# Kernel tuning notes

Measured on AMD Instinct MI355X. Metric: run time of the kernel, lower is better.

The kernel has to match this reference:

```python
import jax, jax.numpy as jnp
import numpy as np


def _block_causal_mask(cu_seqlens, seq_len):
    """Boolean [seq_len, seq_len] mask: True = attend (same doc AND causal)."""
    positions = jnp.arange(seq_len)
    # searchsorted(side='right') - 1 maps each position to its document id
    seq_ids = jnp.searchsorted(cu_seqlens, positions, side='right') - 1
    same_seq = seq_ids[:, None] == seq_ids[None, :]
    causal = positions[None, :] <= positions[:, None]
    return same_seq & causal


def setup_inputs() -> dict:
    key = jax.random.key(0)
    kq, kk, kv, kc = jax.random.split(key, 4)
    B, H, S, D = 1, 16, 4096, 128
    q = jax.random.normal(kq, (B, H, S, D), dtype=jnp.float32)
    k = jax.random.normal(kk, (B, H, S, D), dtype=jnp.float32)
    v = jax.random.normal(kv, (B, H, S, D), dtype=jnp.float32)
    # 8 packed documents: interior boundaries are sorted random ints in (0, S)
    inner = jnp.sort(jax.random.randint(kc, (7,), 1, S, dtype=jnp.int64))
    cu_seqlens = jnp.concatenate([
        jnp.zeros((1,), jnp.int64), inner, jnp.full((1,), S, jnp.int64)
    ])
    return {"q": q, "k": k, "v": v, "cu_seqlens": cu_seqlens, "max_seqlen": S}


def reference(q, k, v, cu_seqlens, max_seqlen):
    # q, k, v: [B, H, S, D]; block-diagonal causal SDPA over packed sequences.
    S, D = q.shape[2], q.shape[3]
    scale = 1.0 / jnp.sqrt(jnp.asarray(D, q.dtype))
    allow = _block_causal_mask(cu_seqlens, S)  # [S, S] bool
    scores = jnp.einsum('bhsd,bhtd->bhst', q, k) * scale  # [B, H, S, S]
    neg_inf = jnp.asarray(-jnp.inf, scores.dtype)
    scores = jnp.where(allow[None, None], scores, neg_inf)
    probs = jax.nn.softmax(scores, axis=-1)
    return jnp.einsum('bhst,bhtd->bhsd', probs, v)
```

## Files before the change

kernel.cpp:

```cpp
#include <hip/hip_runtime.h>

typedef float  f32x4  __attribute__((ext_vector_type(4)));
typedef __bf16 bf16x8 __attribute__((ext_vector_type(8)));
typedef unsigned short u16;
typedef u16 u16x8 __attribute__((ext_vector_type(8)));
typedef u16 u16x4 __attribute__((ext_vector_type(4)));
typedef unsigned u32x4 __attribute__((ext_vector_type(4)));

#define HEADS 16
#define DIM   128
#define QT    64
#define KTILE 64
#define PSTR  72
#define KSTR  136
#define VSTR  68

__device__ __forceinline__ u16 f2bf(float f) {
    unsigned u = __builtin_bit_cast(unsigned, f);
    u += 0x7FFFu + ((u >> 16) & 1u);
    return (u16)(u >> 16);
}

__device__ __forceinline__ void dma16(const void* g, void* l) {
    auto* gp = (const __attribute__((address_space(1))) unsigned*)(uintptr_t)g;
    auto* lp = (__attribute__((address_space(3))) unsigned*)(uintptr_t)l;
    __builtin_amdgcn_global_load_lds(gp, lp, 16, 0, 0);
}

__device__ __forceinline__ unsigned cvtpk(float lo, float hi) {
    unsigned r;
    asm("v_cvt_pk_bf16_f32 %0, %1, %2" : "=v"(r) : "v"(lo), "v"(hi));
    return r;
}

__global__ __launch_bounds__(256) void prep_kv(
    const float* __restrict__ K, const float* __restrict__ V,
    u16* __restrict__ KB, u16* __restrict__ VB, int S)
{
    __shared__ __align__(16) u16 T[128 * 72];
    int nt = S >> 6;
    int tile = blockIdx.x % nt, h = blockIdx.x / nt;
    int t = threadIdx.x;
    long tb = (long)(h * nt + tile) * 8192;

    const float* ksrc = K + ((long)(h * S + tile * 64)) * DIM;
#pragma unroll
    for (int it = 0; it < 4; ++it) {
        int idx = t + it * 256;
        int g = idx & 15, r = idx >> 4;
        const float* src = ksrc + (long)r * DIM + g * 8;
        f32x4 a = *(const f32x4*)src;
        f32x4 b = *(const f32x4*)(src + 4);
        u16x8 o;
        o[0]=f2bf(a[0]); o[1]=f2bf(a[1]); o[2]=f2bf(a[2]); o[3]=f2bf(a[3]);
        o[4]=f2bf(b[0]); o[5]=f2bf(b[1]); o[6]=f2bf(b[2]); o[7]=f2bf(b[3]);
        *(u16x8*)&KB[tb + r * 128 + ((g ^ (r & 7)) << 3)] = o;
    }

    int col4 = (t & 31) * 4;
    int row  = t >> 5;
    const float* vsrc = V + ((long)(h * S + tile * 64)) * DIM;
#pragma unroll
    for (int it = 0; it < 8; ++it) {
        int k = row + it * 8;
        f32x4 x = *(const f32x4*)(vsrc + (long)k * DIM + col4);
        T[(col4 + 0) * 72 + k] = f2bf(x[0]);
        T[(col4 + 1) * 72 + k] = f2bf(x[1]);
        T[(col4 + 2) * 72 + k] = f2bf(x[2]);
        T[(col4 + 3) * 72 + k] = f2bf(x[3]);
    }
    __syncthreads();
#pragma unroll
    for (int it = 0; it < 4; ++it) {
        int idx = t + it * 256;
        int d = idx >> 3, g2 = idx & 7;
        u16x8 o = *(const u16x8*)&T[d * 72 + g2 * 8];
        *(u16x8*)&VB[tb + d * 64 + ((g2 ^ (d & 7)) << 3)] = o;
    }
}

__global__ __launch_bounds__(256, 2) void fa_main(
    const float* __restrict__ Q, const u16* __restrict__ KB,
    const u16* __restrict__ VB, const void* __restrict__ cu_raw,
    int n_cu, float* __restrict__ O, int S, int n_qb)
{
    __shared__ __align__(16) u16 Kb[2][64 * 128];
    __shared__ __align__(16) u16 Vt[2][128 * 64];
    __shared__ __align__(16) u16 On[16 * 64];
    __shared__ int cu_s[32];

    const int tid  = threadIdx.x;
    const int wave = tid >> 6, lane = tid & 63;
    const int quad = lane >> 4, l16 = lane & 15;
    const int h  = blockIdx.x & (HEADS - 1);
    const int qb = (n_qb - 1) - (blockIdx.x >> 4);
    const int q0 = qb * QT;

    {
        const int* cu32 = (const int*)cu_raw;
        bool is64 = (cu32[1] == 0);
        for (int t = tid; t < n_cu; t += blockDim.x)
            cu_s[t] = is64 ? (int)((const long long*)cu_raw)[t] : cu32[t];
    }
    for (int i = tid; i < 1024; i += 256)
        On[i] = (i < 64) ? (u16)0x3F80 : (u16)0;
    __syncthreads();

    const float sc2 = 0.08838834764831845f * 1.4426950408889634f;
    const long hb = (long)h * S * DIM;
    const long hk = (long)h * (S >> 6) * 8192;
    const int qend = q0 + QT;

    const int qi_l = q0 + wave * 16 + l16;
    int qs = 0;
    for (int j = 0; j < n_cu; ++j) if (cu_s[j] <= qi_l) qs = cu_s[j];
    int q0s = 0;
    for (int j = 0; j < n_cu; ++j) if (cu_s[j] <= q0) q0s = cu_s[j];

    bf16x8 qfrag[4];
    {
        const float* qp = Q + hb + (long)(q0 + wave * 16 + l16) * DIM + quad * 8;
#pragma unroll
        for (int kk = 0; kk < 4; ++kk) {
            f32x4 x = *(const f32x4*)(qp + kk * 32);
            f32x4 y = *(const f32x4*)(qp + kk * 32 + 4);
            u16x8 u;
            u[0]=f2bf(x[0]); u[1]=f2bf(x[1]); u[2]=f2bf(x[2]); u[3]=f2bf(x[3]);
            u[4]=f2bf(y[0]); u[5]=f2bf(y[1]); u[6]=f2bf(y[2]); u[7]=f2bf(y[3]);
            qfrag[kk] = __builtin_bit_cast(bf16x8, u);
        }
    }

    f32x4 acc[9];
#pragma unroll
    for (int dt = 0; dt < 9; ++dt) acc[dt] = (f32x4){0.f, 0.f, 0.f, 0.f};

    const int t0 = (q0s & ~(KTILE - 1)) >> 6;
    const int ntile = (qend >> 6) - t0;
    const u16* ksrc = KB + hk;
    const u16* vsrc = VB + hk;

    {
        long off = (long)t0 * 8192;
#pragma unroll
        for (int c = 0; c < 4; ++c) {
            int ch = wave * 4 + c;
            dma16(ksrc + off + ch * 512 + lane * 8, &Kb[0][ch * 512]);
            dma16(vsrc + off + ch * 512 + lane * 8, &Vt[0][ch * 512]);
        }
    }

    for (int i = 0; i < ntile; ++i) {
        const int cur = i & 1;
        if (i + 1 < ntile) {
            long off = (long)(t0 + i + 1) * 8192;
#pragma unroll
            for (int c = 0; c < 4; ++c) {
                int ch = wave * 4 + c;
                dma16(ksrc + off + ch * 512 + lane * 8, &Kb[cur ^ 1][ch * 512]);
                dma16(vsrc + off + ch * 512 + lane * 8, &Vt[cur ^ 1][ch * 512]);
            }
            asm volatile("s_waitcnt vmcnt(8)" ::: "memory");
        } else {
            asm volatile("s_waitcnt vmcnt(0)" ::: "memory");
        }
        __builtin_amdgcn_s_barrier();

        const int kt = (t0 + i) << 6;
        const u16* kb = &Kb[cur][0];
        const u16* vt = &Vt[cur][0];

        f32x4 sc[4];
#pragma unroll
        for (int nt = 0; nt < 4; ++nt) sc[nt] = (f32x4){0.f, 0.f, 0.f, 0.f};
        __builtin_amdgcn_s_setprio(1);
#pragma unroll
        for (int kk = 0; kk < 4; ++kk)
#pragma unroll
            for (int nt = 0; nt < 4; ++nt) {
                int row = nt * 16 + l16;
                int g = kk * 4 + quad;
                u16x8 bu = *(const u16x8*)&kb[row * 128 + ((g ^ (row & 7)) << 3)];
                sc[nt] = __builtin_amdgcn_mfma_f32_16x16x32_bf16(
                    __builtin_bit_cast(bf16x8, bu), qfrag[kk], sc[nt], 0, 0, 0);
            }
        __builtin_amdgcn_s_setprio(0);

        float p[4][4];
#pragma unroll
        for (int nt = 0; nt < 4; ++nt) {
#pragma unroll
            for (int r = 0; r < 4; ++r) {
                int kj = kt + nt * 16 + quad * 4 + r;
                bool ok = (kj >= qs) && (kj <= qi_l);
                p[nt][r] = ok ? __builtin_amdgcn_exp2f(sc[nt][r] * sc2) : 0.f;
            }
        }

        unsigned Ra[4], Rb[4];
#pragma unroll
        for (int nt = 0; nt < 4; ++nt) {
            Ra[nt] = cvtpk(p[nt][0], p[nt][1]);
            Rb[nt] = cvtpk(p[nt][2], p[nt][3]);
        }

        __builtin_amdgcn_s_setprio(1);
#pragma unroll
        for (int kk2 = 0; kk2 < 2; ++kk2) {
            unsigned a0 = Ra[2*kk2], a1 = Ra[2*kk2 + 1];
            unsigned b0 = Rb[2*kk2], b1 = Rb[2*kk2 + 1];
            asm("v_permlane32_swap_b32 %0, %1" : "+v"(a0), "+v"(a1));
            asm("v_permlane16_swap_b32 %0, %1" : "+v"(a0), "+v"(a1));
            asm("v_permlane32_swap_b32 %0, %1" : "+v"(b0), "+v"(b1));
            asm("v_permlane16_swap_b32 %0, %1" : "+v"(b0), "+v"(b1));
            u32x4 wv; wv[0] = a0; wv[1] = b0; wv[2] = a1; wv[3] = b1;
            bf16x8 ap = __builtin_bit_cast(bf16x8, wv);

            int g2 = kk2 * 4 + quad;
#pragma unroll
            for (int dt = 0; dt < 8; ++dt) {
                int d = dt * 16 + l16;
                u16x8 bu = *(const u16x8*)&vt[(d << 6) + ((g2 ^ (d & 7)) << 3)];
                acc[dt] = __builtin_amdgcn_mfma_f32_16x16x32_bf16(
                    ap, __builtin_bit_cast(bf16x8, bu), acc[dt], 0, 0, 0);
            }
            {
                u16x8 bo = *(const u16x8*)&On[(l16 << 6) + ((g2 ^ (l16 & 7)) << 3)];
                acc[8] = __builtin_amdgcn_mfma_f32_16x16x32_bf16(
                    ap, __builtin_bit_cast(bf16x8, bo), acc[8], 0, 0, 0);
            }
        }
        __builtin_amdgcn_s_setprio(0);

        __builtin_amdgcn_s_barrier();
    }

#pragma unroll
    for (int r = 0; r < 4; ++r) {
        float l = __shfl(acc[8][r], (lane & 48), 64);
        int qi = q0 + wave * 16 + quad * 4 + r;
        float inv = 1.f / l;
        float* op = O + hb + (long)qi * DIM + l16;
#pragma unroll
        for (int dt = 0; dt < 8; ++dt)
            op[dt * 16] = acc[dt][r] * inv;
    }
}

__global__ __launch_bounds__(256, 2) void fa_fallback(
    const float* __restrict__ Q, const float* __restrict__ K,
    const float* __restrict__ V, const void* __restrict__ cu_raw,
    int n_cu, float* __restrict__ O, int S)
{
    __shared__ __align__(16) u16 Kb[KTILE * KSTR];
    __shared__ __align__(16) u16 Vt[DIM * VSTR];
    __shared__ __align__(16) u16 Pw[4][16 * PSTR];
    __shared__ int cu_s[32];

    const int tid  = threadIdx.x;
    const int wave = tid >> 6, lane = tid & 63;
    const int quad = lane >> 4, l16 = lane & 15;
    const int q0   = blockIdx.x * QT;
    const int h    = blockIdx.y;
    const int cg = tid & 31, rr = tid >> 5;
    const int dv = tid & 127, hiv = tid >> 7;

    {
        const int* cu32 = (const int*)cu_raw;
        bool is64 = (cu32[1] == 0);
        for (int t = tid; t < n_cu; t += blockDim.x)
            cu_s[t] = is64 ? (int)((const long long*)cu_raw)[t] : cu32[t];
    }
    __syncthreads();

    const long hb = (long)h * S * DIM;
    const float NEG_INF = -__builtin_inff();
    const float scale = 0.08838834764831845f;

    int qstart[4];
#pragma unroll
    for (int r = 0; r < 4; ++r) {
        int qi = q0 + wave * 16 + quad * 4 + r;
        int st = 0;
        for (int j = 0; j < n_cu; ++j) if (cu_s[j] <= qi) st = cu_s[j];
        qstart[r] = st;
    }
    int q0s = 0;
    for (int j = 0; j < n_cu; ++j) if (cu_s[j] <= q0) q0s = cu_s[j];

    bf16x8 qfrag[4];
    {
        const float* qp = Q + hb + (long)(q0 + wave * 16 + l16) * DIM + quad * 8;
#pragma unroll
        for (int kk = 0; kk < 4; ++kk) {
            f32x4 x = *(const f32x4*)(qp + kk * 32);
            f32x4 y = *(const f32x4*)(qp + kk * 32 + 4);
            u16x8 u;
            u[0]=f2bf(x[0]); u[1]=f2bf(x[1]); u[2]=f2bf(x[2]); u[3]=f2bf(x[3]);
            u[4]=f2bf(y[0]); u[5]=f2bf(y[1]); u[6]=f2bf(y[2]); u[7]=f2bf(y[3]);
            qfrag[kk] = __builtin_bit_cast(bf16x8, u);
        }
    }

    f32x4 acc[8];
#pragma unroll
    for (int dt = 0; dt < 8; ++dt) acc[dt] = (f32x4){0.f, 0.f, 0.f, 0.f};
    float m_r[4], l_r[4];
#pragma unroll
    for (int r = 0; r < 4; ++r) { m_r[r] = NEG_INF; l_r[r] = 0.f; }

    for (int kt = q0s & ~(KTILE - 1); kt < q0 + QT; kt += KTILE) {
        __syncthreads();
        {
#pragma unroll
            for (int it = 0; it < 8; ++it) {
                f32x4 kx = *(const f32x4*)(K + hb + (long)(kt + rr + it*8) * DIM + cg*4);
                u16x4 kb4;
                kb4[0]=f2bf(kx[0]); kb4[1]=f2bf(kx[1]);
                kb4[2]=f2bf(kx[2]); kb4[3]=f2bf(kx[3]);
                *(u16x4*)&Kb[(rr + it*8) * KSTR + cg*4] = kb4;
            }
#pragma unroll
            for (int p = 0; p < 8; ++p) {
                int kq = 2*p + hiv;
                const float* vp = V + hb + (long)(kt + kq*4) * DIM + dv;
                u16x4 w;
                w[0]=f2bf(vp[0]); w[1]=f2bf(vp[(long)DIM]);
                w[2]=f2bf(vp[(long)2*DIM]); w[3]=f2bf(vp[(long)3*DIM]);
                *(u16x4*)&Vt[dv * VSTR + kq*4] = w;
            }
        }
        __syncthreads();

        f32x4 sc[4];
#pragma unroll
        for (int nt = 0; nt < 4; ++nt) sc[nt] = (f32x4){0.f, 0.f, 0.f, 0.f};
#pragma unroll
        for (int kk = 0; kk < 4; ++kk)
#pragma unroll
            for (int nt = 0; nt < 4; ++nt) {
                u16x8 bu = *(const u16x8*)&Kb[(nt*16 + l16) * KSTR + kk*32 + quad*8];
                sc[nt] = __builtin_amdgcn_mfma_f32_16x16x32_bf16(
                    qfrag[kk], __builtin_bit_cast(bf16x8, bu), sc[nt], 0, 0, 0);
            }
#pragma unroll
        for (int nt = 0; nt < 4; ++nt) {
            int kj = kt + nt * 16 + l16;
#pragma unroll
            for (int r = 0; r < 4; ++r) {
                int qi = q0 + wave * 16 + quad * 4 + r;
                bool ok = (kj >= qstart[r]) && (kj <= qi);
                sc[nt][r] = ok ? sc[nt][r] * scale : NEG_INF;
            }
        }
        float mnew[4], alpha[4], rsum[4];
#pragma unroll
        for (int r = 0; r < 4; ++r) {
            float tm = fmaxf(fmaxf(sc[0][r], sc[1][r]), fmaxf(sc[2][r], sc[3][r]));
#pragma unroll
            for (int off = 1; off < 16; off <<= 1)
                tm = fmaxf(tm, __shfl_xor(tm, off, 64));
            float mn = fmaxf(m_r[r], tm);
            mnew[r]  = mn;
            alpha[r] = (mn == NEG_INF) ? 1.f : __expf(m_r[r] - mn);
            rsum[r]  = 0.f;
        }
#pragma unroll
        for (int nt = 0; nt < 4; ++nt)
#pragma unroll
            for (int r = 0; r < 4; ++r) {
                float pv = (sc[nt][r] == NEG_INF) ? 0.f : __expf(sc[nt][r] - mnew[r]);
                sc[nt][r] = pv;
                rsum[r] += pv;
            }
#pragma unroll
        for (int r = 0; r < 4; ++r) {
            float s = rsum[r];
#pragma unroll
            for (int off = 1; off < 16; off <<= 1) s += __shfl_xor(s, off, 64);
            l_r[r] = l_r[r] * alpha[r] + s;
            m_r[r] = mnew[r];
        }
#pragma unroll
        for (int dt = 0; dt < 8; ++dt)
#pragma unroll
            for (int r = 0; r < 4; ++r) acc[dt][r] *= alpha[r];

#pragma unroll
        for (int nt = 0; nt < 4; ++nt)
#pragma unroll
            for (int r = 0; r < 4; ++r)
                Pw[wave][(quad*4 + r) * PSTR + ((nt ^ quad) * 16 + l16)] = f2bf(sc[nt][r]);

#pragma unroll
        for (int kk2 = 0; kk2 < 2; ++kk2) {
            int colx = (kk2*32 + quad*8) ^ ((l16 >> 2) << 4);
            u16x8 au = *(const u16x8*)&Pw[wave][l16 * PSTR + colx];
            bf16x8 ap = __builtin_bit_cast(bf16x8, au);
#pragma unroll
            for (int dt = 0; dt < 8; ++dt) {
                int base = (dt*16 + l16) * VSTR + kk2*32 + quad*8;
                u16x4 lo = *(const u16x4*)&Vt[base];
                u16x4 hi = *(const u16x4*)&Vt[base + 4];
                u16x8 bu;
                bu[0]=lo[0]; bu[1]=lo[1]; bu[2]=lo[2]; bu[3]=lo[3];
                bu[4]=hi[0]; bu[5]=hi[1]; bu[6]=hi[2]; bu[7]=hi[3];
                acc[dt] = __builtin_amdgcn_mfma_f32_16x16x32_bf16(
                    ap, __builtin_bit_cast(bf16x8, bu), acc[dt], 0, 0, 0);
            }
        }
    }

#pragma unroll
    for (int r = 0; r < 4; ++r) {
        int qi = q0 + wave * 16 + quad * 4 + r;
        float inv = 1.f / l_r[r];
        float* op = O + hb + (long)qi * DIM + l16;
#pragma unroll
        for (int dt = 0; dt < 8; ++dt)
            op[dt * 16] = acc[dt][r] * inv;
    }
}

extern "C" void kernel_launch(void* const* d_in, const int* in_sizes, int n_in,
                              void* d_out, int out_size, void* d_ws, size_t ws_size,
                              hipStream_t stream) {
    const float* q = (const float*)d_in[0];
    const float* k = (const float*)d_in[1];
    const float* v = (const float*)d_in[2];
    const void* cu = d_in[3];
    int n_cu = in_sizes[3];
    int S = in_sizes[0] / (HEADS * DIM);
    size_t perMat = (size_t)HEADS * S * 256;
    if (ws_size >= 2 * perMat) {
        u16* KB = (u16*)d_ws;
        u16* VB = (u16*)((char*)d_ws + perMat);
        prep_kv<<<dim3(HEADS * (S >> 6)), 256, 0, stream>>>(k, v, KB, VB, S);
        int n_qb = S / QT;
        fa_main<<<dim3(n_qb * HEADS), 256, 0, stream>>>(
            q, KB, VB, cu, n_cu, (float*)d_out, S, n_qb);
    } else {
        fa_fallback<<<dim3(S / QT, HEADS), 256, 0, stream>>>(
            q, k, v, cu, n_cu, (float*)d_out, S);
    }
}
```

Measured before the change: 174.8 us.

## Double query tile per block to reuse K/V tiles across two row groups

Each wave now handles two 16-row query groups (128 query rows per block), so every K and V fragment read from LDS feeds two MFMAs instead of one. This halves K/V staging per query row and the number of blocks. Blocks are remapped so each of the 8 XCDs gets a fixed pair of heads, which should improve L2 locality. The row-sum ones matrix moves from LDS into a register constant. Costs are higher register pressure, fewer blocks (512) for load balance across the causal triangle, and a coarser causal start tile.

Result: slower. 187.6 us (+7.3%).

```diff
diff --git a/kernel.cpp b/kernel.cpp
--- a/kernel.cpp
+++ b/kernel.cpp
@@ -9,6 +9,7 @@
 
 #define HEADS 16
 #define DIM   128
+#define QTM   128
 #define QT    64
 #define KTILE 64
 #define PSTR  72
@@ -86,15 +87,26 @@
 {
     __shared__ __align__(16) u16 Kb[2][64 * 128];
     __shared__ __align__(16) u16 Vt[2][128 * 64];
-    __shared__ __align__(16) u16 On[16 * 64];
     __shared__ int cu_s[32];
 
     const int tid  = threadIdx.x;
     const int wave = tid >> 6, lane = tid & 63;
     const int quad = lane >> 4, l16 = lane & 15;
-    const int h  = blockIdx.x & (HEADS - 1);
-    const int qb = (n_qb - 1) - (blockIdx.x >> 4);
-    const int q0 = qb * QT;
+
+    int h, qb;
+    {
+        int total = n_qb * HEADS;
+        int bid = blockIdx.x;
+        if ((total & 7) == 0) {
+            int xcd = bid & 7, j = bid >> 3;
+            h  = xcd * (HEADS >> 3) + (j & ((HEADS >> 3) - 1));
+            qb = (n_qb - 1) - (j >> 1);
+        } else {
+            h  = bid & (HEADS - 1);
+            qb = (n_qb - 1) - (bid / HEADS);
+        }
+    }
+    const int q0 = qb * QTM;
 
     {
         const int* cu32 = (const int*)cu_raw;
@@ -102,24 +114,28 @@
         for (int t = tid; t < n_cu; t += blockDim.x)
             cu_s[t] = is64 ? (int)((const long long*)cu_raw)[t] : cu32[t];
     }
-    for (int i = tid; i < 1024; i += 256)
-        On[i] = (i < 64) ? (u16)0x3F80 : (u16)0;
     __syncthreads();
 
     const float sc2 = 0.08838834764831845f * 1.4426950408889634f;
     const long hb = (long)h * S * DIM;
     const long hk = (long)h * (S >> 6) * 8192;
-    const int qend = q0 + QT;
-
-    const int qi_l = q0 + wave * 16 + l16;
-    int qs = 0;
-    for (int j = 0; j < n_cu; ++j) if (cu_s[j] <= qi_l) qs = cu_s[j];
+    const int qend = q0 + QTM;
+
+    int qi_l[2], qs[2];
+#pragma unroll
+    for (int m = 0; m < 2; ++m) {
+        qi_l[m] = q0 + wave * 32 + m * 16 + l16;
+        int st = 0;
+        for (int j = 0; j < n_cu; ++j) if (cu_s[j] <= qi_l[m]) st = cu_s[j];
+        qs[m] = st;
+    }
     int q0s = 0;
     for (int j = 0; j < n_cu; ++j) if (cu_s[j] <= q0) q0s = cu_s[j];
 
-    bf16x8 qfrag[4];
-    {
-        const float* qp = Q + hb + (long)(q0 + wave * 16 + l16) * DIM + quad * 8;
+    bf16x8 qfrag[2][4];
+#pragma unroll
+    for (int m = 0; m < 2; ++m) {
+        const float* qp = Q + hb + (long)qi_l[m] * DIM + quad * 8;
 #pragma unroll
         for (int kk = 0; kk < 4; ++kk) {
             f32x4 x = *(const f32x4*)(qp + kk * 32);
@@ -127,13 +143,24 @@
             u16x8 u;
             u[0]=f2bf(x[0]); u[1]=f2bf(x[1]); u[2]=f2bf(x[2]); u[3]=f2bf(x[3]);
             u[4]=f2bf(y[0]); u[5]=f2bf(y[1]); u[6]=f2bf(y[2]); u[7]=f2bf(y[3]);
-            qfrag[kk] = __builtin_bit_cast(bf16x8, u);
-        }
-    }
-
-    f32x4 acc[9];
-#pragma unroll
-    for (int dt = 0; dt < 9; ++dt) acc[dt] = (f32x4){0.f, 0.f, 0.f, 0.f};
+            qfrag[m][kk] = __builtin_bit_cast(bf16x8, u);
+        }
+    }
+
+    bf16x8 ones;
+    {
+        u16 ov = (l16 == 0) ? (u16)0x3F80 : (u16)0;
+        u16x8 ou;
+#pragma unroll
+        for (int j = 0; j < 8; ++j) ou[j] = ov;
+        ones = __builtin_bit_cast(bf16x8, ou);
+    }
+
+    f32x4 acc[2][9];
+#pragma unroll
+    for (int m = 0; m < 2; ++m)
+#pragma unroll
+        for (int dt = 0; dt < 9; ++dt) acc[m][dt] = (f32x4){0.f, 0.f, 0.f, 0.f};
 
     const int t0 = (q0s & ~(KTILE - 1)) >> 6;
     const int ntile = (qend >> 6) - t0;
@@ -170,9 +197,11 @@
         const u16* kb = &Kb[cur][0];
         const u16* vt = &Vt[cur][0];
 
-        f32x4 sc[4];
-#pragma unroll
-        for (int nt = 0; nt < 4; ++nt) sc[nt] = (f32x4){0.f, 0.f, 0.f, 0.f};
+        f32x4 sc[2][4];
+#pragma unroll
+        for (int m = 0; m < 2; ++m)
+#pragma unroll
+            for (int nt = 0; nt < 4; ++nt) sc[m][nt] = (f32x4){0.f, 0.f, 0.f, 0.f};
         __builtin_amdgcn_s_setprio(1);
 #pragma unroll
         for (int kk = 0; kk < 4; ++kk)
@@ -181,54 +210,62 @@
                 int row = nt * 16 + l16;
                 int g = kk * 4 + quad;
                 u16x8 bu = *(const u16x8*)&kb[row * 128 + ((g ^ (row & 7)) << 3)];
-                sc[nt] = __builtin_amdgcn_mfma_f32_16x16x32_bf16(
-                    __builtin_bit_cast(bf16x8, bu), qfrag[kk], sc[nt], 0, 0, 0);
+                bf16x8 kf = __builtin_bit_cast(bf16x8, bu);
+                sc[0][nt] = __builtin_amdgcn_mfma_f32_16x16x32_bf16(
+                    kf, qfrag[0][kk], sc[0][nt], 0, 0, 0);
+                sc[1][nt] = __builtin_amdgcn_mfma_f32_16x16x32_bf16(
+                    kf, qfrag[1][kk], sc[1][nt], 0, 0, 0);
             }
         __builtin_amdgcn_s_setprio(0);
 
-        float p[4][4];
-#pragma unroll
-        for (int nt = 0; nt < 4; ++nt) {
-#pragma unroll
-            for (int r = 0; r < 4; ++r) {
-                int kj = kt + nt * 16 + quad * 4 + r;
-                bool ok = (kj >= qs) && (kj <= qi_l);
-                p[nt][r] = ok ? __builtin_amdgcn_exp2f(sc[nt][r] * sc2) : 0.f;
-            }
-        }
-
-        unsigned Ra[4], Rb[4];
-#pragma unroll
-        for (int nt = 0; nt < 4; ++nt) {
-            Ra[nt] = cvtpk(p[nt][0], p[nt][1]);
-            Rb[nt] = cvtpk(p[nt][2], p[nt][3]);
-        }
+        unsigned Ra[2][4], Rb[2][4];
+#pragma unroll
+        for (int m = 0; m < 2; ++m)
+#pragma unroll
+            for (int nt = 0; nt < 4; ++nt) {
+                int kjb = kt + nt * 16 + quad * 4;
+                float p0 = (kjb + 0 >= qs[m] && kjb + 0 <= qi_l[m])
+                               ? __builtin_amdgcn_exp2f(sc[m][nt][0] * sc2) : 0.f;
+                float p1 = (kjb + 1 >= qs[m] && kjb + 1 <= qi_l[m])
+                               ? __builtin_amdgcn_exp2f(sc[m][nt][1] * sc2) : 0.f;
+                float p2 = (kjb + 2 >= qs[m] && kjb + 2 <= qi_l[m])
+                               ? __builtin_amdgcn_exp2f(sc[m][nt][2] * sc2) : 0.f;
+                float p3 = (kjb + 3 >= qs[m] && kjb + 3 <= qi_l[m])
+                               ? __builtin_amdgcn_exp2f(sc[m][nt][3] * sc2) : 0.f;
+                Ra[m][nt] = cvtpk(p0, p1);
+                Rb[m][nt] = cvtpk(p2, p3);
+            }
 
         __builtin_amdgcn_s_setprio(1);
 #pragma unroll
         for (int kk2 = 0; kk2 < 2; ++kk2) {
-            unsigned a0 = Ra[2*kk2], a1 = Ra[2*kk2 + 1];
-            unsigned b0 = Rb[2*kk2], b1 = Rb[2*kk2 + 1];
-            asm("v_permlane32_swap_b32 %0, %1" : "+v"(a0), "+v"(a1));
-            asm("v_permlane16_swap_b32 %0, %1" : "+v"(a0), "+v"(a1));
-            asm("v_permlane32_swap_b32 %0, %1" : "+v"(b0), "+v"(b1));
-            asm("v_permlane16_swap_b32 %0, %1" : "+v"(b0), "+v"(b1));
-            u32x4 wv; wv[0] = a0; wv[1] = b0; wv[2] = a1; wv[3] = b1;
-            bf16x8 ap = __builtin_bit_cast(bf16x8, wv);
-
+            bf16x8 ap[2];
+#pragma unroll
+            for (int m = 0; m < 2; ++m) {
+                unsigned a0 = Ra[m][2*kk2], a1 = Ra[m][2*kk2 + 1];
+                unsigned b0 = Rb[m][2*kk2], b1 = Rb[m][2*kk2 + 1];
+                asm("v_permlane32_swap_b32 %0, %1" : "+v"(a0), "+v"(a1));
+                asm("v_permlane16_swap_b32 %0, %1" : "+v"(a0), "+v"(a1));
+                asm("v_permlane32_swap_b32 %0, %1" : "+v"(b0), "+v"(b1));
+                asm("v_permlane16_swap_b32 %0, %1" : "+v"(b0), "+v"(b1));
+                u32x4 wv; wv[0] = a0; wv[1] = b0; wv[2] = a1; wv[3] = b1;
+                ap[m] = __builtin_bit_cast(bf16x8, wv);
+            }
             int g2 = kk2 * 4 + quad;
 #pragma unroll
             for (int dt = 0; dt < 8; ++dt) {
                 int d = dt * 16 + l16;
                 u16x8 bu = *(const u16x8*)&vt[(d << 6) + ((g2 ^ (d & 7)) << 3)];
-                acc[dt] = __builtin_amdgcn_mfma_f32_16x16x32_bf16(
-                    ap, __builtin_bit_cast(bf16x8, bu), acc[dt], 0, 0, 0);
-            }
-            {
-                u16x8 bo = *(const u16x8*)&On[(l16 << 6) + ((g2 ^ (l16 & 7)) << 3)];
-                acc[8] = __builtin_amdgcn_mfma_f32_16x16x32_bf16(
-                    ap, __builtin_bit_cast(bf16x8, bo), acc[8], 0, 0, 0);
-            }
+                bf16x8 vf = __builtin_bit_cast(bf16x8, bu);
+                acc[0][dt] = __builtin_amdgcn_mfma_f32_16x16x32_bf16(
+                    ap[0], vf, acc[0][dt], 0, 0, 0);
+                acc[1][dt] = __builtin_amdgcn_mfma_f32_16x16x32_bf16(
+                    ap[1], vf, acc[1][dt], 0, 0, 0);
+            }
+            acc[0][8] = __builtin_amdgcn_mfma_f32_16x16x32_bf16(
+                ap[0], ones, acc[0][8], 0, 0, 0);
+            acc[1][8] = __builtin_amdgcn_mfma_f32_16x16x32_bf16(
+                ap[1], ones, acc[1][8], 0, 0, 0);
         }
         __builtin_amdgcn_s_setprio(0);
 
@@ -236,14 +273,16 @@
     }
 
 #pragma unroll
+    for (int m = 0; m < 2; ++m)
+#pragma unroll
     for (int r = 0; r < 4; ++r) {
-        float l = __shfl(acc[8][r], (lane & 48), 64);
-        int qi = q0 + wave * 16 + quad * 4 + r;
+        float l = __shfl(acc[m][8][r], (lane & 48), 64);
+        int qi = q0 + wave * 32 + m * 16 + quad * 4 + r;
         float inv = 1.f / l;
         float* op = O + hb + (long)qi * DIM + l16;
 #pragma unroll
         for (int dt = 0; dt < 8; ++dt)
-            op[dt * 16] = acc[dt][r] * inv;
+            op[dt * 16] = acc[m][dt][r] * inv;
     }
 }
 
@@ -432,11 +471,11 @@
     int n_cu = in_sizes[3];
     int S = in_sizes[0] / (HEADS * DIM);
     size_t perMat = (size_t)HEADS * S * 256;
-    if (ws_size >= 2 * perMat) {
+    if (ws_size >= 2 * perMat && (S % QTM) == 0) {
         u16* KB = (u16*)d_ws;
         u16* VB = (u16*)((char*)d_ws + perMat);
         prep_kv<<<dim3(HEADS * (S >> 6)), 256, 0, stream>>>(k, v, KB, VB, S);
-        int n_qb = S / QT;
+        int n_qb = S / QTM;
         fa_main<<<dim3(n_qb * HEADS), 256, 0, stream>>>(
             q, KB, VB, cu, n_cu, (float*)d_out, S, n_qb);
     } else {
```

## Single-buffer V, drop On LDS table, skip masked tiles, remap blocks per XCD

Applied to the files above, without the earlier changes.

V is now single-buffered in LDS and the LDS row-sum table is replaced with a register 'ones' fragment. Together these cut shared memory so the launch bound can rise to 3 blocks per CU. The V load for the next tile is issued after the barrier, so only K stays double-buffered. Waves skip the compute for tiles entirely outside their document/causal range. The block-to-(head, q-block) mapping is remapped so each XCD handles two heads, which should improve L2 locality. The trade-off is that V loads are less overlapped with compute.

New measurement: 179.3 us. 1.03x slower.

```diff
diff --git a/kernel.cpp b/kernel.cpp
--- a/kernel.cpp
+++ b/kernel.cpp
@@ -79,21 +79,32 @@
     }
 }
 
-__global__ __launch_bounds__(256, 2) void fa_main(
+__global__ __launch_bounds__(256, 3) void fa_main(
     const float* __restrict__ Q, const u16* __restrict__ KB,
     const u16* __restrict__ VB, const void* __restrict__ cu_raw,
     int n_cu, float* __restrict__ O, int S, int n_qb)
 {
     __shared__ __align__(16) u16 Kb[2][64 * 128];
-    __shared__ __align__(16) u16 Vt[2][128 * 64];
-    __shared__ __align__(16) u16 On[16 * 64];
+    __shared__ __align__(16) u16 Vt[128 * 64];
     __shared__ int cu_s[32];
 
     const int tid  = threadIdx.x;
     const int wave = tid >> 6, lane = tid & 63;
     const int quad = lane >> 4, l16 = lane & 15;
-    const int h  = blockIdx.x & (HEADS - 1);
-    const int qb = (n_qb - 1) - (blockIdx.x >> 4);
+
+    int h, qb;
+    {
+        int bid = blockIdx.x;
+        int total = n_qb * HEADS;
+        if ((total & 15) == 0) {
+            int xcd = bid & 7, j = bid >> 3;
+            h  = xcd * 2 + (j & 1);
+            qb = (n_qb - 1) - (j >> 1);
+        } else {
+            h  = bid & (HEADS - 1);
+            qb = (n_qb - 1) - (bid >> 4);
+        }
+    }
     const int q0 = qb * QT;
 
     {
@@ -102,8 +113,6 @@
         for (int t = tid; t < n_cu; t += blockDim.x)
             cu_s[t] = is64 ? (int)((const long long*)cu_raw)[t] : cu32[t];
     }
-    for (int i = tid; i < 1024; i += 256)
-        On[i] = (i < 64) ? (u16)0x3F80 : (u16)0;
     __syncthreads();
 
     const float sc2 = 0.08838834764831845f * 1.4426950408889634f;
@@ -117,9 +126,12 @@
     int q0s = 0;
     for (int j = 0; j < n_cu; ++j) if (cu_s[j] <= q0) q0s = cu_s[j];
 
+    const int wqmin = __builtin_amdgcn_readfirstlane(qs);
+    const int wqmax = q0 + wave * 16 + 15;
+
     bf16x8 qfrag[4];
     {
-        const float* qp = Q + hb + (long)(q0 + wave * 16 + l16) * DIM + quad * 8;
+        const float* qp = Q + hb + (long)qi_l * DIM + quad * 8;
 #pragma unroll
         for (int kk = 0; kk < 4; ++kk) {
             f32x4 x = *(const f32x4*)(qp + kk * 32);
@@ -131,6 +143,15 @@
         }
     }
 
+    bf16x8 ones;
+    {
+        u16 ov = (l16 == 0) ? (u16)0x3F80 : (u16)0;
+        u16x8 ou;
+#pragma unroll
+        for (int j = 0; j < 8; ++j) ou[j] = ov;
+        ones = __builtin_bit_cast(bf16x8, ou);
+    }
+
     f32x4 acc[9];
 #pragma unroll
     for (int dt = 0; dt < 9; ++dt) acc[dt] = (f32x4){0.f, 0.f, 0.f, 0.f};
@@ -146,7 +167,7 @@
         for (int c = 0; c < 4; ++c) {
             int ch = wave * 4 + c;
             dma16(ksrc + off + ch * 512 + lane * 8, &Kb[0][ch * 512]);
-            dma16(vsrc + off + ch * 512 + lane * 8, &Vt[0][ch * 512]);
+            dma16(vsrc + off + ch * 512 + lane * 8, &Vt[ch * 512]);
         }
     }
 
@@ -158,81 +179,84 @@
             for (int c = 0; c < 4; ++c) {
                 int ch = wave * 4 + c;
                 dma16(ksrc + off + ch * 512 + lane * 8, &Kb[cur ^ 1][ch * 512]);
-                dma16(vsrc + off + ch * 512 + lane * 8, &Vt[cur ^ 1][ch * 512]);
-            }
-            asm volatile("s_waitcnt vmcnt(8)" ::: "memory");
+            }
+            asm volatile("s_waitcnt vmcnt(4)" ::: "memory");
         } else {
             asm volatile("s_waitcnt vmcnt(0)" ::: "memory");
         }
         __builtin_amdgcn_s_barrier();
 
         const int kt = (t0 + i) << 6;
-        const u16* kb = &Kb[cur][0];
-        const u16* vt = &Vt[cur][0];
-
-        f32x4 sc[4];
-#pragma unroll
-        for (int nt = 0; nt < 4; ++nt) sc[nt] = (f32x4){0.f, 0.f, 0.f, 0.f};
-        __builtin_amdgcn_s_setprio(1);
-#pragma unroll
-        for (int kk = 0; kk < 4; ++kk)
+        if (kt <= wqmax && kt + KTILE > wqmin) {
+            const u16* kb = &Kb[cur][0];
+
+            f32x4 sc[4];
+#pragma unroll
+            for (int nt = 0; nt < 4; ++nt) sc[nt] = (f32x4){0.f, 0.f, 0.f, 0.f};
+            __builtin_amdgcn_s_setprio(1);
+#pragma unroll
+            for (int kk = 0; kk < 4; ++kk)
+#pragma unroll
+                for (int nt = 0; nt < 4; ++nt) {
+                    int row = nt * 16 + l16;
+                    int g = kk * 4 + quad;
+                    u16x8 bu = *(const u16x8*)&kb[row * 128 + ((g ^ (row & 7)) << 3)];
+                    sc[nt] = __builtin_amdgcn_mfma_f32_16x16x32_bf16(
+                        __builtin_bit_cast(bf16x8, bu), qfrag[kk], sc[nt], 0, 0, 0);
+                }
+            __builtin_amdgcn_s_setprio(0);
+
+            unsigned Ra[4], Rb[4];
 #pragma unroll
             for (int nt = 0; nt < 4; ++nt) {
-                int row = nt * 16 + l16;
-                int g = kk * 4 + quad;
-                u16x8 bu = *(const u16x8*)&kb[row * 128 + ((g ^ (row & 7)) << 3)];
-                sc[nt] = __builtin_amdgcn_mfma_f32_16x16x32_bf16(
-                    __builtin_bit_cast(bf16x8, bu), qfrag[kk], sc[nt], 0, 0, 0);
-            }
-        __builtin_amdgcn_s_setprio(0);
-
-        float p[4][4];
-#pragma unroll
-        for (int nt = 0; nt < 4; ++nt) {
-#pragma unroll
-            for (int r = 0; r < 4; ++r) {
-                int kj = kt + nt * 16 + quad * 4 + r;
-                bool ok = (kj >= qs) && (kj <= qi_l);
-                p[nt][r] = ok ? __builtin_amdgcn_exp2f(sc[nt][r] * sc2) : 0.f;
-            }
-        }
-
-        unsigned Ra[4], Rb[4];
-#pragma unroll
-        for (int nt = 0; nt < 4; ++nt) {
-            Ra[nt] = cvtpk(p[nt][0], p[nt][1]);
-            Rb[nt] = cvtpk(p[nt][2], p[nt][3]);
-        }
-
-        __builtin_amdgcn_s_setprio(1);
-#pragma unroll
-        for (int kk2 = 0; kk2 < 2; ++kk2) {
-            unsigned a0 = Ra[2*kk2], a1 = Ra[2*kk2 + 1];
-            unsigned b0 = Rb[2*kk2], b1 = Rb[2*kk2 + 1];
-            asm("v_permlane32_swap_b32 %0, %1" : "+v"(a0), "+v"(a1));
-            asm("v_permlane16_swap_b32 %0, %1" : "+v"(a0), "+v"(a1));
-            asm("v_permlane32_swap_b32 %0, %1" : "+v"(b0), "+v"(b1));
-            asm("v_permlane16_swap_b32 %0, %1" : "+v"(b0), "+v"(b1));
-            u32x4 wv; wv[0] = a0; wv[1] = b0; wv[2] = a1; wv[3] = b1;
-            bf16x8 ap = __builtin_bit_cast(bf16x8, wv);
-
-            int g2 = kk2 * 4 + quad;
-#pragma unroll
-            for (int dt = 0; dt < 8; ++dt) {
-                int d = dt * 16 + l16;
-                u16x8 bu = *(const u16x8*)&vt[(d << 6) + ((g2 ^ (d & 7)) << 3)];
-                acc[dt] = __builtin_amdgcn_mfma_f32_16x16x32_bf16(
-                    ap, __builtin_bit_cast(bf16x8, bu), acc[dt], 0, 0, 0);
-            }
-            {
-                u16x8 bo = *(const u16x8*)&On[(l16 << 6) + ((g2 ^ (l16 & 7)) << 3)];
+                int kjb = kt + nt * 16 + quad * 4;
+                float p0 = (kjb + 0 >= qs && kjb + 0 <= qi_l)
+                               ? __builtin_amdgcn_exp2f(sc[nt][0] * sc2) : 0.f;
+                float p1 = (kjb + 1 >= qs && kjb + 1 <= qi_l)
+                               ? __builtin_amdgcn_exp2f(sc[nt][1] * sc2) : 0.f;
+                float p2 = (kjb + 2 >= qs && kjb + 2 <= qi_l)
+                               ? __builtin_amdgcn_exp2f(sc[nt][2] * sc2) : 0.f;
+                float p3 = (kjb + 3 >= qs && kjb + 3 <= qi_l)
+                               ? __builtin_amdgcn_exp2f(sc[nt][3] * sc2) : 0.f;
+                Ra[nt] = cvtpk(p0, p1);
+                Rb[nt] = cvtpk(p2, p3);
+            }
+
+            __builtin_amdgcn_s_setprio(1);
+#pragma unroll
+            for (int kk2 = 0; kk2 < 2; ++kk2) {
+                unsigned a0 = Ra[2*kk2], a1 = Ra[2*kk2 + 1];
+                unsigned b0 = Rb[2*kk2], b1 = Rb[2*kk2 + 1];
+                asm("v_permlane32_swap_b32 %0, %1" : "+v"(a0), "+v"(a1));
+                asm("v_permlane16_swap_b32 %0, %1" : "+v"(a0), "+v"(a1));
+                asm("v_permlane32_swap_b32 %0, %1" : "+v"(b0), "+v"(b1));
+                asm("v_permlane16_swap_b32 %0, %1" : "+v"(b0), "+v"(b1));
+                u32x4 wv; wv[0] = a0; wv[1] = b0; wv[2] = a1; wv[3] = b1;
+                bf16x8 ap = __builtin_bit_cast(bf16x8, wv);
+
+                int g2 = kk2 * 4 + quad;
+#pragma unroll
+                for (int dt = 0; dt < 8; ++dt) {
+                    int d = dt * 16 + l16;
+                    u16x8 bu = *(const u16x8*)&Vt[(d << 6) + ((g2 ^ (d & 7)) << 3)];
+                    acc[dt] = __builtin_amdgcn_mfma_f32_16x16x32_bf16(
+                        ap, __builtin_bit_cast(bf16x8, bu), acc[dt], 0, 0, 0);
+                }
                 acc[8] = __builtin_amdgcn_mfma_f32_16x16x32_bf16(
-                    ap, __builtin_bit_cast(bf16x8, bo), acc[8], 0, 0, 0);
-            }
-        }
-        __builtin_amdgcn_s_setprio(0);
+                    ap, ones, acc[8], 0, 0, 0);
+            }
+            __builtin_amdgcn_s_setprio(0);
+        }
 
         __builtin_amdgcn_s_barrier();
+        if (i + 1 < ntile) {
+            long off = (long)(t0 + i + 1) * 8192;
+#pragma unroll
+            for (int c = 0; c < 4; ++c) {
+                int ch = wave * 4 + c;
+                dma16(vsrc + off + ch * 512 + lane * 8, &Vt[ch * 512]);
+            }
+        }
     }
 
 #pragma unroll
```

## Interleave QK MFMA with exp2 masking and hold ones-vector in registers

Applied to the files above, without the earlier changes.

Reorders the QK^T loop so that each 16-column score tile is finished first, then computes the exp2, mask and bf16 pack for the previous tile while the next tile's MFMAs issue. This overlaps transcendental and VALU work with matrix ops. It also replaces the LDS-resident ones matrix used for the row-sum MFMA with a register constant, which removes an LDS read per step and the LDS allocation. The mask check becomes a single unsigned range compare. The softmax has no max subtraction, so the accuracy behaviour is unchanged.

Result: no change. 172.0 us (-1.6%).

```diff
diff --git a/kernel.cpp b/kernel.cpp
--- a/kernel.cpp
+++ b/kernel.cpp
@@ -86,7 +86,6 @@
 {
     __shared__ __align__(16) u16 Kb[2][64 * 128];
     __shared__ __align__(16) u16 Vt[2][128 * 64];
-    __shared__ __align__(16) u16 On[16 * 64];
     __shared__ int cu_s[32];
 
     const int tid  = threadIdx.x;
@@ -102,8 +101,6 @@
         for (int t = tid; t < n_cu; t += blockDim.x)
             cu_s[t] = is64 ? (int)((const long long*)cu_raw)[t] : cu32[t];
     }
-    for (int i = tid; i < 1024; i += 256)
-        On[i] = (i < 64) ? (u16)0x3F80 : (u16)0;
     __syncthreads();
 
     const float sc2 = 0.08838834764831845f * 1.4426950408889634f;
@@ -116,10 +113,11 @@
     for (int j = 0; j < n_cu; ++j) if (cu_s[j] <= qi_l) qs = cu_s[j];
     int q0s = 0;
     for (int j = 0; j < n_cu; ++j) if (cu_s[j] <= q0) q0s = cu_s[j];
+    const int drange = qi_l - qs;
 
     bf16x8 qfrag[4];
     {
-        const float* qp = Q + hb + (long)(q0 + wave * 16 + l16) * DIM + quad * 8;
+        const float* qp = Q + hb + (long)qi_l * DIM + quad * 8;
 #pragma unroll
         for (int kk = 0; kk < 4; ++kk) {
             f32x4 x = *(const f32x4*)(qp + kk * 32);
@@ -131,6 +129,15 @@
         }
     }
 
+    bf16x8 ones;
+    {
+        u16 ov = (l16 == 0) ? (u16)0x3F80 : (u16)0;
+        u16x8 ou;
+#pragma unroll
+        for (int j = 0; j < 8; ++j) ou[j] = ov;
+        ones = __builtin_bit_cast(bf16x8, ou);
+    }
+
     f32x4 acc[9];
 #pragma unroll
     for (int dt = 0; dt < 9; ++dt) acc[dt] = (f32x4){0.f, 0.f, 0.f, 0.f};
@@ -171,40 +178,42 @@
         const u16* vt = &Vt[cur][0];
 
         f32x4 sc[4];
+        unsigned Ra[4], Rb[4];
+        const int base0 = (kt - qs) + quad * 4;
 #pragma unroll
         for (int nt = 0; nt < 4; ++nt) sc[nt] = (f32x4){0.f, 0.f, 0.f, 0.f};
+
+#define EXP2N(n)                                                              \
+        {                                                                     \
+            int b_ = base0 + (n) * 16;                                        \
+            float p0 = ((unsigned)(b_ + 0) <= (unsigned)drange)               \
+                           ? __builtin_amdgcn_exp2f(sc[n][0] * sc2) : 0.f;    \
+            float p1 = ((unsigned)(b_ + 1) <= (unsigned)drange)               \
+                           ? __builtin_amdgcn_exp2f(sc[n][1] * sc2) : 0.f;    \
+            float p2 = ((unsigned)(b_ + 2) <= (unsigned)drange)               \
+                           ? __builtin_amdgcn_exp2f(sc[n][2] * sc2) : 0.f;    \
+            float p3 = ((unsigned)(b_ + 3) <= (unsigned)drange)               \
+                           ? __builtin_amdgcn_exp2f(sc[n][3] * sc2) : 0.f;    \
+            Ra[n] = cvtpk(p0, p1);                                            \
+            Rb[n] = cvtpk(p2, p3);                                            \
+        }
+
         __builtin_amdgcn_s_setprio(1);
 #pragma unroll
-        for (int kk = 0; kk < 4; ++kk)
-#pragma unroll
-            for (int nt = 0; nt < 4; ++nt) {
+        for (int nt = 0; nt < 4; ++nt) {
+#pragma unroll
+            for (int kk = 0; kk < 4; ++kk) {
                 int row = nt * 16 + l16;
                 int g = kk * 4 + quad;
                 u16x8 bu = *(const u16x8*)&kb[row * 128 + ((g ^ (row & 7)) << 3)];
                 sc[nt] = __builtin_amdgcn_mfma_f32_16x16x32_bf16(
                     __builtin_bit_cast(bf16x8, bu), qfrag[kk], sc[nt], 0, 0, 0);
             }
-        __builtin_amdgcn_s_setprio(0);
-
-        float p[4][4];
-#pragma unroll
-        for (int nt = 0; nt < 4; ++nt) {
-#pragma unroll
-            for (int r = 0; r < 4; ++r) {
-                int kj = kt + nt * 16 + quad * 4 + r;
-                bool ok = (kj >= qs) && (kj <= qi_l);
-                p[nt][r] = ok ? __builtin_amdgcn_exp2f(sc[nt][r] * sc2) : 0.f;
-            }
-        }
-
-        unsigned Ra[4], Rb[4];
-#pragma unroll
-        for (int nt = 0; nt < 4; ++nt) {
-            Ra[nt] = cvtpk(p[nt][0], p[nt][1]);
-            Rb[nt] = cvtpk(p[nt][2], p[nt][3]);
-        }
-
-        __builtin_amdgcn_s_setprio(1);
+            if (nt >= 1) EXP2N(nt - 1);
+        }
+        EXP2N(3);
+#undef EXP2N
+
 #pragma unroll
         for (int kk2 = 0; kk2 < 2; ++kk2) {
             unsigned a0 = Ra[2*kk2], a1 = Ra[2*kk2 + 1];
@@ -224,11 +233,8 @@
                 acc[dt] = __builtin_amdgcn_mfma_f32_16x16x32_bf16(
                     ap, __builtin_bit_cast(bf16x8, bu), acc[dt], 0, 0, 0);
             }
-            {
-                u16x8 bo = *(const u16x8*)&On[(l16 << 6) + ((g2 ^ (l16 & 7)) << 3)];
-                acc[8] = __builtin_amdgcn_mfma_f32_16x16x32_bf16(
-                    ap, __builtin_bit_cast(bf16x8, bo), acc[8], 0, 0, 0);
-            }
+            acc[8] = __builtin_amdgcn_mfma_f32_16x16x32_bf16(
+                ap, ones, acc[8], 0, 0, 0);
         }
         __builtin_amdgcn_s_setprio(0);
 
```
